# Kernel tuning notes

Measured on AMD Instinct MI355X. Metric: run time of the kernel, lower is better.

The kernel has to match this reference:

```python
import jax, jax.numpy as jnp
import numpy as np

B, S, E, H = 4, 8192, 1024, 16
D = E // H  # head_dim = 64


def setup_inputs() -> dict:
    key = jax.random.key(0)
    ks = jax.random.split(key, 6)
    x = jax.random.normal(ks[0], (B, S, E), dtype=jnp.float32)
    key_padding_mask = jax.random.randint(ks[1], (B, S), 0, 2).astype(jnp.bool_)
    scale = 1.0 / np.sqrt(E)
    Wq = jax.random.normal(ks[2], (E, E), dtype=jnp.float32) * scale
    Wk = jax.random.normal(ks[3], (E, E), dtype=jnp.float32) * scale
    Wv = jax.random.normal(ks[4], (E, E), dtype=jnp.float32) * scale
    Wo = jax.random.normal(ks[5], (E, E), dtype=jnp.float32) * scale
    return {"x": x, "key_padding_mask": key_padding_mask,
            "Wq": Wq, "Wk": Wk, "Wv": Wv, "Wo": Wo}


def reference(x, key_padding_mask, Wq, Wk, Wv, Wo):
    b, s, _ = x.shape
    # torch Linear (no bias): y = x @ W.T
    Q = (x @ Wq.T).reshape(b, s, H, D).transpose(0, 2, 1, 3)  # (b,h,s,d)
    K = (x @ Wk.T).reshape(b, s, H, D).transpose(0, 2, 1, 3)
    V = (x @ Wv.T).reshape(b, s, H, D).transpose(0, 2, 1, 3)
    Q = jax.nn.elu(Q) + 1.0
    K = jax.nn.elu(K) + 1.0
    mask = key_padding_mask[:, None, :, None]  # (b,1,s,1), True = padding
    K = jnp.where(mask, 0.0, K)
    V = jnp.where(mask, 0.0, V)
    # global KV summarization over sequence: (b,h,d,e)
    KV = jnp.einsum('bhsd,bhse->bhde', K, V)
    K_sum = K.sum(axis=2)  # (b,h,d)
    Z = 1.0 / (jnp.einsum('bhsd,bhd->bhs', Q, K_sum) + 1e-6)  # (b,h,s)
    out = jnp.einsum('bhsd,bhde->bhse', Q, KV) * Z[..., None]  # (b,h,s,e)
    out = out.transpose(0, 2, 1, 3).reshape(b, s, E)
    return out @ Wo.T
```

## Files before the change

kernel.cpp:

```cpp
#include <hip/hip_runtime.h>

#define NB 4
#define NS 8192
#define NE 1024
#define NH 16
#define ND 64
#define NM (NB*NS)
#define NKT 16

typedef __bf16 bf16x8 __attribute__((ext_vector_type(8)));
typedef float  f32x4  __attribute__((ext_vector_type(4)));
typedef unsigned short u16x8 __attribute__((ext_vector_type(8)));

__device__ __forceinline__ unsigned short f2bf(float f){
  unsigned int u = __float_as_uint(f);
  u += 0x7FFFu + ((u >> 16) & 1u);
  return (unsigned short)(u >> 16);
}
__device__ __forceinline__ float bf2f(unsigned short h){
  return __uint_as_float(((unsigned int)h) << 16);
}
__device__ __forceinline__ void gload16(const void* g, void* lds){
  __builtin_amdgcn_global_load_lds(
      (__attribute__((address_space(1))) unsigned int*)g,
      (__attribute__((address_space(3))) unsigned int*)lds, 16, 0, 0);
}

__global__ void mask_prep(const void* mraw, unsigned char* mask_u8){
  __shared__ int flag_s;
  if (threadIdx.x == 0) flag_s = 0;
  __syncthreads();
  const unsigned int* mi = (const unsigned int*)mraw;
  int bad = 0;
  for (int i = threadIdx.x; i < 4096; i += 256) bad |= (mi[i] > 1u) ? 1 : 0;
  if (bad) atomicOr(&flag_s, 1);
  __syncthreads();
  const int isbyte = flag_s;
  const unsigned char* mb = (const unsigned char*)mraw;
  int stride = gridDim.x * blockDim.x;
  for (int i = blockIdx.x*blockDim.x + threadIdx.x; i < NM; i += stride)
    mask_u8[i] = isbyte ? (unsigned char)(mb[i] != 0) : (unsigned char)(mi[i] != 0);
}

struct CastJobs {
  const float* src[5];
  unsigned short* dst[5];
  int n4[5];
};

__global__ __launch_bounds__(256) void castk(CastJobs J){
  int j = blockIdx.y;
  const float* s = J.src[j];
  unsigned short* d = J.dst[j];
  int n4 = J.n4[j];
  int stride = gridDim.x * blockDim.x;
  for (int i = blockIdx.x*blockDim.x + threadIdx.x; i < n4; i += stride){
    float4 v = *(const float4*)(s + (long)i*4);
    ushort4 o;
    o.x = f2bf(v.x); o.y = f2bf(v.y); o.z = f2bf(v.z); o.w = f2bf(v.w);
    *(ushort4*)(d + (long)i*4) = o;
  }
}

__global__ __launch_bounds__(512, 2) void gemm256(
    const unsigned short* __restrict__ A,
    const unsigned short* __restrict__ W1,
    const unsigned short* __restrict__ W2,
    unsigned short* __restrict__ O1,
    unsigned short* __restrict__ O2,
    float* __restrict__ OF,
    const unsigned char* __restrict__ mask,
    int modeSel)
{
  __shared__ __align__(16) unsigned short As[2*256*64];
  __shared__ __align__(16) unsigned short Bs[2*256*64];

  const int mode = (modeSel < 0) ? (int)blockIdx.y + 1 : modeSel;
  const unsigned short* Bw = (mode==1) ? W1 : (mode==2) ? W2 : W1;
  unsigned short* Obf = (mode==1) ? O1 : O2;

  const int nwg = (int)gridDim.x;
  const int bx  = (int)blockIdx.x;
  const int swz = (bx & 7) * (nwg >> 3) + (bx >> 3);
  const long m0 = (long)(swz >> 2) * 256;
  const int  n0 = (swz & 3) * 256;

  const int tid = (int)threadIdx.x;
  const int l   = tid & 63;
  const int wv  = tid >> 6;
  const int wr  = wv >> 2;
  const int wc  = wv & 3;
  const int l15 = l & 15;
  const int lhi = l >> 4;
  const int swz8 = (l & 7) * 8;

  const int srow = wv*16 + (l >> 3);
  const int scol = ((l & 7) * 8) ^ ((l >> 3) << 3);

  auto stageA = [&](int st, int h){
    if (st >= NKT) return;
    const long col = (long)st*64 + scol;
    #pragma unroll
    for (int is = 0; is < 2; ++is)
      gload16(A + (m0 + h*128 + srow + is*8)*NE + col,
              &As[(st & 1)*16384 + h*8192 + (wv*2 + is)*512]);
  };
  auto stageB = [&](int st, int h){
    if (st >= NKT) return;
    const long col = (long)st*64 + scol;
    #pragma unroll
    for (int is = 0; is < 2; ++is)
      gload16(Bw + (long)(n0 + h*128 + srow + is*8)*NE + col,
              &Bs[(st & 1)*16384 + h*8192 + (wv*2 + is)*512]);
  };

  auto lda = [&](int buf, int mi, int ks)->bf16x8 {
    const int row = wr*128 + mi*16 + l15;
    const int col = (ks*32 + lhi*8) ^ swz8;
    return *(const bf16x8*)&As[buf*16384 + row*64 + col];
  };
  auto ldb = [&](int buf, int ni, int ks)->bf16x8 {
    const int row = wc*64 + ni*16 + l15;
    const int col = (ks*32 + lhi*8) ^ swz8;
    return *(const bf16x8*)&Bs[buf*16384 + row*64 + col];
  };

  f32x4 acc[8][4];
  #pragma unroll
  for (int i=0;i<8;++i)
    #pragma unroll
    for (int j=0;j<4;++j)
      acc[i][j] = (f32x4){0.f,0.f,0.f,0.f};

  stageA(0,0); stageA(0,1); stageB(0,0); stageB(0,1);
  stageA(1,0); stageA(1,1); stageB(1,0); stageB(1,1);
  asm volatile("s_waitcnt vmcnt(8)" ::: "memory");
  __builtin_amdgcn_s_barrier();

  bf16x8 a0[4][2], a1[4][2], b0[2][2], b1[2][2];

  #pragma unroll 2
  for (int kt = 0; kt < NKT; ++kt){
    const int buf = kt & 1;

    #pragma unroll
    for (int i=0;i<4;++i){ a0[i][0]=lda(buf,i,0); a0[i][1]=lda(buf,i,1); }
    #pragma unroll
    for (int j=0;j<2;++j){ b0[j][0]=ldb(buf,j,0); b0[j][1]=ldb(buf,j,1); }
    asm volatile("s_waitcnt lgkmcnt(0)" ::: "memory");
    __builtin_amdgcn_sched_barrier(0);
    __builtin_amdgcn_s_setprio(1);
    #pragma unroll
    for (int ks=0;ks<2;++ks)
      #pragma unroll
      for (int i=0;i<4;++i)
        #pragma unroll
        for (int j=0;j<2;++j)
          acc[i][j] = __builtin_amdgcn_mfma_f32_16x16x32_bf16(a0[i][ks], b0[j][ks], acc[i][j], 0,0,0);
    __builtin_amdgcn_s_setprio(0);
    __builtin_amdgcn_s_barrier();

    #pragma unroll
    for (int i=0;i<4;++i){ a1[i][0]=lda(buf,4+i,0); a1[i][1]=lda(buf,4+i,1); }
    asm volatile("s_waitcnt lgkmcnt(0)" ::: "memory");
    __builtin_amdgcn_sched_barrier(0);
    __builtin_amdgcn_s_setprio(1);
    #pragma unroll
    for (int ks=0;ks<2;++ks)
      #pragma unroll
      for (int i=0;i<4;++i)
        #pragma unroll
        for (int j=0;j<2;++j)
          acc[4+i][j] = __builtin_amdgcn_mfma_f32_16x16x32_bf16(a1[i][ks], b0[j][ks], acc[4+i][j], 0,0,0);
    __builtin_amdgcn_s_setprio(0);
    __builtin_amdgcn_s_barrier();

    #pragma unroll
    for (int j=0;j<2;++j){ b1[j][0]=ldb(buf,2+j,0); b1[j][1]=ldb(buf,2+j,1); }
    stageA(kt+2, 0); stageA(kt+2, 1);
    asm volatile("s_waitcnt lgkmcnt(0)" ::: "memory");
    __builtin_amdgcn_sched_barrier(0);
    __builtin_amdgcn_s_setprio(1);
    #pragma unroll
    for (int ks=0;ks<2;++ks)
      #pragma unroll
      for (int i=0;i<4;++i)
        #pragma unroll
        for (int j=0;j<2;++j)
          acc[4+i][2+j] = __builtin_amdgcn_mfma_f32_16x16x32_bf16(a1[i][ks], b1[j][ks], acc[4+i][2+j], 0,0,0);
    __builtin_amdgcn_s_setprio(0);
    __builtin_amdgcn_s_barrier();

    stageB(kt+2, 0); stageB(kt+2, 1);
    __builtin_amdgcn_sched_barrier(0);
    __builtin_amdgcn_s_setprio(1);
    #pragma unroll
    for (int ks=0;ks<2;++ks)
      #pragma unroll
      for (int i=0;i<4;++i)
        #pragma unroll
        for (int j=0;j<2;++j)
          acc[i][2+j] = __builtin_amdgcn_mfma_f32_16x16x32_bf16(a0[i][ks], b1[j][ks], acc[i][2+j], 0,0,0);
    __builtin_amdgcn_s_setprio(0);
    if (kt < NKT-2)       asm volatile("s_waitcnt vmcnt(8)" ::: "memory");
    else if (kt == NKT-2) asm volatile("s_waitcnt vmcnt(0)" ::: "memory");
    __builtin_amdgcn_s_barrier();
  }

  #pragma unroll
  for (int mi=0;mi<8;++mi){
    #pragma unroll
    for (int r=0;r<4;++r){
      const long mg = m0 + wr*128 + mi*16 + lhi*4 + r;
      const bool mz = (mode==1 || mode==2) ? (mask[mg] != 0) : false;
      #pragma unroll
      for (int ni=0;ni<4;++ni){
        const int ng = n0 + wc*64 + ni*16 + l15;
        float v = acc[mi][ni][r];
        if (mode==1) v = (v > 0.f) ? (v + 1.f) : __expf(v);
        if (mz) v = 0.f;
        if (mode==3) OF[mg*NE + ng] = v;
        else         Obf[mg*NE + ng] = f2bf(v);
      }
    }
  }
}

__global__ __launch_bounds__(512, 2) void gemm_q_attn(
    const unsigned short* __restrict__ A,
    const unsigned short* __restrict__ Wq,
    const unsigned short* __restrict__ KVfrag,
    unsigned short* __restrict__ attnb)
{
  __shared__ __align__(16) unsigned short As[2*256*64];
  __shared__ __align__(16) unsigned short Bs[2*256*64];

  const int nwg = (int)gridDim.x;
  const int bx  = (int)blockIdx.x;
  const int swz = (bx & 7) * (nwg >> 3) + (bx >> 3);
  const long m0 = (long)(swz >> 2) * 256;
  const int  n0 = (swz & 3) * 256;

  const int tid = (int)threadIdx.x;
  const int l   = tid & 63;
  const int wv  = tid >> 6;
  const int wr  = wv >> 2;
  const int wc  = wv & 3;
  const int l15 = l & 15;
  const int lhi = l >> 4;
  const int swz8 = (l & 7) * 8;

  const int srow = wv*16 + (l >> 3);
  const int scol = ((l & 7) * 8) ^ ((l >> 3) << 3);

  auto stageA = [&](int st, int h){
    if (st >= NKT) return;
    const long col = (long)st*64 + scol;
    #pragma unroll
    for (int is = 0; is < 2; ++is)
      gload16(A + (m0 + h*128 + srow + is*8)*NE + col,
              &As[(st & 1)*16384 + h*8192 + (wv*2 + is)*512]);
  };
  auto stageB = [&](int st, int h){
    if (st >= NKT) return;
    const long col = (long)st*64 + scol;
    #pragma unroll
    for (int is = 0; is < 2; ++is)
      gload16(Wq + (long)(n0 + h*128 + srow + is*8)*NE + col,
              &Bs[(st & 1)*16384 + h*8192 + (wv*2 + is)*512]);
  };

  auto lda = [&](int buf, int mi, int ks)->bf16x8 {
    const int row = wr*128 + mi*16 + l15;
    const int col = (ks*32 + lhi*8) ^ swz8;
    return *(const bf16x8*)&As[buf*16384 + row*64 + col];
  };
  auto ldb = [&](int buf, int ni, int ks)->bf16x8 {
    const int row = wc*64 + ni*16 + l15;
    const int col = (ks*32 + lhi*8) ^ swz8;
    return *(const bf16x8*)&Bs[buf*16384 + row*64 + col];
  };

  f32x4 acc[8][4];
  #pragma unroll
  for (int i=0;i<8;++i)
    #pragma unroll
    for (int j=0;j<4;++j)
      acc[i][j] = (f32x4){0.f,0.f,0.f,0.f};

  stageA(0,0); stageA(0,1); stageB(0,0); stageB(0,1);
  stageA(1,0); stageA(1,1); stageB(1,0); stageB(1,1);
  asm volatile("s_waitcnt vmcnt(8)" ::: "memory");
  __builtin_amdgcn_s_barrier();

  bf16x8 a0[4][2], a1[4][2], b0[2][2], b1[2][2];

  #pragma unroll 2
  for (int kt = 0; kt < NKT; ++kt){
    const int buf = kt & 1;

    #pragma unroll
    for (int i=0;i<4;++i){ a0[i][0]=lda(buf,i,0); a0[i][1]=lda(buf,i,1); }
    #pragma unroll
    for (int j=0;j<2;++j){ b0[j][0]=ldb(buf,j,0); b0[j][1]=ldb(buf,j,1); }
    asm volatile("s_waitcnt lgkmcnt(0)" ::: "memory");
    __builtin_amdgcn_sched_barrier(0);
    __builtin_amdgcn_s_setprio(1);
    #pragma unroll
    for (int ks=0;ks<2;++ks)
      #pragma unroll
      for (int i=0;i<4;++i)
        #pragma unroll
        for (int j=0;j<2;++j)
          acc[i][j] = __builtin_amdgcn_mfma_f32_16x16x32_bf16(a0[i][ks], b0[j][ks], acc[i][j], 0,0,0);
    __builtin_amdgcn_s_setprio(0);
    __builtin_amdgcn_s_barrier();

    #pragma unroll
    for (int i=0;i<4;++i){ a1[i][0]=lda(buf,4+i,0); a1[i][1]=lda(buf,4+i,1); }
    asm volatile("s_waitcnt lgkmcnt(0)" ::: "memory");
    __builtin_amdgcn_sched_barrier(0);
    __builtin_amdgcn_s_setprio(1);
    #pragma unroll
    for (int ks=0;ks<2;++ks)
      #pragma unroll
      for (int i=0;i<4;++i)
        #pragma unroll
        for (int j=0;j<2;++j)
          acc[4+i][j] = __builtin_amdgcn_mfma_f32_16x16x32_bf16(a1[i][ks], b0[j][ks], acc[4+i][j], 0,0,0);
    __builtin_amdgcn_s_setprio(0);
    __builtin_amdgcn_s_barrier();

    #pragma unroll
    for (int j=0;j<2;++j){ b1[j][0]=ldb(buf,2+j,0); b1[j][1]=ldb(buf,2+j,1); }
    stageA(kt+2, 0); stageA(kt+2, 1);
    asm volatile("s_waitcnt lgkmcnt(0)" ::: "memory");
    __builtin_amdgcn_sched_barrier(0);
    __builtin_amdgcn_s_setprio(1);
    #pragma unroll
    for (int ks=0;ks<2;++ks)
      #pragma unroll
      for (int i=0;i<4;++i)
        #pragma unroll
        for (int j=0;j<2;++j)
          acc[4+i][2+j] = __builtin_amdgcn_mfma_f32_16x16x32_bf16(a1[i][ks], b1[j][ks], acc[4+i][2+j], 0,0,0);
    __builtin_amdgcn_s_setprio(0);
    __builtin_amdgcn_s_barrier();

    stageB(kt+2, 0); stageB(kt+2, 1);
    __builtin_amdgcn_sched_barrier(0);
    __builtin_amdgcn_s_setprio(1);
    #pragma unroll
    for (int ks=0;ks<2;++ks)
      #pragma unroll
      for (int i=0;i<4;++i)
        #pragma unroll
        for (int j=0;j<2;++j)
          acc[i][2+j] = __builtin_amdgcn_mfma_f32_16x16x32_bf16(a0[i][ks], b1[j][ks], acc[i][2+j], 0,0,0);
    __builtin_amdgcn_s_setprio(0);
    if (kt < NKT-2)       asm volatile("s_waitcnt vmcnt(8)" ::: "memory");
    else if (kt == NKT-2) asm volatile("s_waitcnt vmcnt(0)" ::: "memory");
    __builtin_amdgcn_s_barrier();
  }

  const int b  = (int)(m0 >> 13);
  const int h  = (swz & 3)*4 + wc;
  const long bh = (long)(b*16 + h);
  unsigned short* pool = (wv < 4) ? &As[wv*8192] : &Bs[(wv-4)*8192];

  #pragma unroll
  for (int mi=0;mi<8;++mi){
    #pragma unroll
    for (int r=0;r<4;++r){
      const int row = mi*16 + lhi*4 + r;
      #pragma unroll
      for (int ni=0;ni<4;++ni){
        float v = acc[mi][ni][r];
        v = (v > 0.f) ? (v + 1.f) : __expf(v);
        const int colb = (ni*16 + l15)*2;
        *(unsigned short*)((char*)pool + row*128 + (colb ^ ((row & 7) << 4))) = f2bf(v);
      }
    }
  }

  bf16x8 bfv[4][5];
  #pragma unroll
  for (int ks=0; ks<4; ++ks)
    #pragma unroll
    for (int nt=0; nt<5; ++nt)
      bfv[ks][nt] = *(const bf16x8*)(KVfrag + bh*10240 + (ks*5+nt)*512 + l*8);

  asm volatile("s_waitcnt lgkmcnt(0)" ::: "memory");
  __builtin_amdgcn_sched_barrier(0);

  const int swzb = (l15 & 7) << 4;
  #pragma unroll
  for (int rt=0; rt<8; ++rt){
    const int rb = (rt*16 + l15)*128;
    bf16x8 qa0 = *(const bf16x8*)((const char*)pool + rb + ((lhi*16) ^ swzb));
    bf16x8 qa1 = *(const bf16x8*)((const char*)pool + rb + ((64 + lhi*16) ^ swzb));
    f32x4 at[5];
    #pragma unroll
    for (int nt=0; nt<5; ++nt){
      at[nt] = (f32x4){0.f,0.f,0.f,0.f};
      at[nt] = __builtin_amdgcn_mfma_f32_16x16x32_bf16(qa0, bfv[0][nt], at[nt], 0,0,0);
      at[nt] = __builtin_amdgcn_mfma_f32_16x16x32_bf16(qa1, bfv[1][nt], at[nt], 0,0,0);
      at[nt] = __builtin_amdgcn_mfma_f32_16x16x32_bf16(qa0, bfv[2][nt], at[nt], 0,0,0);
      at[nt] = __builtin_amdgcn_mfma_f32_16x16x32_bf16(qa1, bfv[3][nt], at[nt], 0,0,0);
    }
    float dv[4];
    #pragma unroll
    for (int e=0;e<4;++e){
      float d = __shfl(at[4][e], l & 48, 64);
      dv[e] = 1.f / (d + 1e-6f);
    }
    #pragma unroll
    for (int nt=0; nt<4; ++nt){
      #pragma unroll
      for (int e=0;e<4;++e){
        const int row = rt*16 + lhi*4 + e;
        const int colb = (nt*16 + l15)*2;
        *(unsigned short*)((char*)pool + row*128 + (colb ^ ((row & 7) << 4))) = f2bf(at[nt][e] * dv[e]);
      }
    }
  }

  asm volatile("s_waitcnt lgkmcnt(0)" ::: "memory");
  __builtin_amdgcn_sched_barrier(0);
  #pragma unroll
  for (int c=0;c<16;++c){
    const int r = c*8 + (l >> 3);
    bf16x8 vv = *(const bf16x8*)((const char*)pool + r*128 + ((((l&7) ^ (r & 7))) << 4));
    *(bf16x8*)(attnb + (m0 + wr*128 + r)*NE + h*ND + (l&7)*8) = vv;
  }
}

__global__ __launch_bounds__(256) void kv_reduce(const unsigned short* __restrict__ K,
                                                 const unsigned short* __restrict__ V,
                                                 float* __restrict__ part){
  __shared__ float lds[2*64*68 + 192];
  float* Ksf = lds;
  float* Vsf = lds + 64*68;
  float* kcorner = lds + 2*64*68;

  const int bid = blockIdx.x;
  const int bh = bid >> 5;
  const int chunk = bid & 31;
  const int b = bh >> 4, h = bh & 15;
  const int t = threadIdx.x, w = t >> 6, l = t & 63;
  const int dg = l & 7, eg = l >> 3;
  const int d0 = dg*8, e0 = eg*8;
  const long base = ((long)b*NS + (long)chunk*256)*NE + h*ND;

  f32x4 acc[8][2];
  #pragma unroll
  for (int j=0;j<8;++j){ acc[j][0]=(f32x4){0,0,0,0}; acc[j][1]=(f32x4){0,0,0,0}; }
  f32x4 ksa = (f32x4){0,0,0,0}, ksb = (f32x4){0,0,0,0};

  for (int sc = 0; sc < 4; ++sc){
    if (sc) __syncthreads();
    const long rbase = base + (long)sc*64*NE;
    #pragma unroll
    for (int p = 0; p < 2; ++p){
      const int g = p*256 + t;
      const int row = g >> 3, cg = (g & 7)*8;
      u16x8 ku = *(const u16x8*)(K + rbase + (long)row*NE + cg);
      u16x8 vu = *(const u16x8*)(V + rbase + (long)row*NE + cg);
      #pragma unroll
      for (int j=0;j<8;++j){
        Ksf[row*68 + cg + j] = bf2f(ku[j]);
        Vsf[row*68 + cg + j] = bf2f(vu[j]);
      }
    }
    __syncthreads();
    #pragma unroll 2
    for (int i = 0; i < 16; ++i){
      const int r = w*16 + i;
      f32x4 k0 = *(const f32x4*)&Ksf[r*68 + d0];
      f32x4 k1 = *(const f32x4*)&Ksf[r*68 + d0 + 4];
      f32x4 v0 = *(const f32x4*)&Vsf[r*68 + e0];
      f32x4 v1 = *(const f32x4*)&Vsf[r*68 + e0 + 4];
      #pragma unroll
      for (int j=0;j<4;++j){
        acc[j][0]   += k0[j]*v0;  acc[j][1]   += k0[j]*v1;
        acc[4+j][0] += k1[j]*v0;  acc[4+j][1] += k1[j]*v1;
      }
      if (eg == 0){ ksa += k0; ksb += k1; }
    }
  }

  __syncthreads();
  if (w >= 1 && eg == 0){
    *(f32x4*)&kcorner[(w-1)*64 + d0]     = ksa;
    *(f32x4*)&kcorner[(w-1)*64 + d0 + 4] = ksb;
  }
  if (w >= 2){
    float* reg = (w==2) ? Ksf : Vsf;
    #pragma unroll
    for (int j=0;j<8;++j)
      #pragma unroll
      for (int q=0;q<2;++q)
        *(f32x4*)&reg[l*68 + (j*2+q)*4] = acc[j][q];
  }
  __syncthreads();
  if (w < 2){
    float* reg = (w==0) ? Ksf : Vsf;
    #pragma unroll
    for (int j=0;j<8;++j)
      #pragma unroll
      for (int q=0;q<2;++q)
        acc[j][q] += *(const f32x4*)&reg[l*68 + (j*2+q)*4];
  }
  __syncthreads();
  if (w == 1){
    #pragma unroll
    for (int j=0;j<8;++j)
      #pragma unroll
      for (int q=0;q<2;++q)
        *(f32x4*)&Ksf[l*68 + (j*2+q)*4] = acc[j][q];
  }
  __syncthreads();
  if (w == 0){
    #pragma unroll
    for (int j=0;j<8;++j)
      #pragma unroll
      for (int q=0;q<2;++q)
        acc[j][q] += *(const f32x4*)&Ksf[l*68 + (j*2+q)*4];
    float* po = part + (long)(bh*32 + chunk)*4160;
    #pragma unroll
    for (int j=0;j<8;++j)
      #pragma unroll
      for (int q=0;q<2;++q)
        *(f32x4*)&po[(d0 + j)*64 + e0 + q*4] = acc[j][q];
    if (eg == 0){
      #pragma unroll
      for (int i=0;i<3;++i){
        ksa += *(const f32x4*)&kcorner[i*64 + d0];
        ksb += *(const f32x4*)&kcorner[i*64 + d0 + 4];
      }
      *(f32x4*)&po[4096 + d0]     = ksa;
      *(f32x4*)&po[4096 + d0 + 4] = ksb;
    }
  }
}

__global__ __launch_bounds__(256) void kv_finish(const float* __restrict__ part,
                                                 unsigned short* __restrict__ KVfrag){
  __shared__ float KVf[64*65 + 32];
  const int bh = blockIdx.x, t = threadIdx.x;
  const float* pb = part + (long)bh*32*4160;

  #pragma unroll
  for (int p = 0; p < 4; ++p){
    int g = p*256 + t;
    f32x4 s = (f32x4){0.f,0.f,0.f,0.f};
    for (int c = 0; c < 32; ++c) s += *(const f32x4*)&pb[c*4160 + g*4];
    int d = g >> 4, e = (g & 15)*4;
    KVf[d*65 + e+0] = s[0];
    KVf[d*65 + e+1] = s[1];
    KVf[d*65 + e+2] = s[2];
    KVf[d*65 + e+3] = s[3];
  }
  if (t < 16){
    f32x4 s = (f32x4){0.f,0.f,0.f,0.f};
    for (int c = 0; c < 32; ++c) s += *(const f32x4*)&pb[c*4160 + 4096 + t*4];
    #pragma unroll
    for (int j=0;j<4;++j) KVf[(t*4+j)*65 + 64] = s[j];
  }
  __syncthreads();

  for (int idx = t; idx < 10240; idx += 256){
    int j   = idx & 7;
    int lfr = (idx >> 3) & 63;
    int grp = idx >> 9;
    int nt  = grp % 5, ks = grp / 5;
    int kk  = (ks & 1)*32 + (lfr >> 4)*8 + j;
    int n   = nt*16 + (lfr & 15);
    float v = (n <= 64) ? KVf[kk*65 + n] : 0.f;
    unsigned short hi = f2bf(v);
    unsigned short o  = (ks >> 1) ? f2bf(v - bf2f(hi)) : hi;
    KVfrag[(long)bh*10240 + idx] = o;
  }
}

extern "C" void kernel_launch(void* const* d_in, const int* in_sizes, int n_in,
                              void* d_out, int out_size, void* d_ws, size_t ws_size,
                              hipStream_t stream){
  (void)in_sizes; (void)n_in; (void)out_size; (void)ws_size;
  const float* x    = (const float*)d_in[0];
  const void*  mraw = d_in[1];
  const float* Wq   = (const float*)d_in[2];
  const float* Wk   = (const float*)d_in[3];
  const float* Wv   = (const float*)d_in[4];
  const float* Wo   = (const float*)d_in[5];
  float* out = (float*)d_out;
  char* ws = (char*)d_ws;

  unsigned short* xb  = (unsigned short*)(ws + 0L);
  unsigned short* Wqb = (unsigned short*)(ws + 67108864L);
  unsigned short* Wkb = (unsigned short*)(ws + 69206016L);
  unsigned short* Wvb = (unsigned short*)(ws + 71303168L);
  unsigned short* Wob = (unsigned short*)(ws + 73400320L);
  unsigned short* Qb  = (unsigned short*)(ws + 75497472L);
  unsigned short* Kb  = (unsigned short*)(ws + 142606336L);
  unsigned short* Vb  = (unsigned short*)(ws + 209715200L);
  unsigned short* KVfrag = (unsigned short*)(ws + 276824064L);
  unsigned char* mask_u8 = (unsigned char*)(ws + 278462464L);
  float* part = (float*)Qb;
  unsigned short* attnb = Qb;

  mask_prep<<<32, 256, 0, stream>>>(mraw, mask_u8);

  CastJobs J;
  J.src[0]=x;  J.dst[0]=xb;  J.n4[0]=NM*NE/4;
  J.src[1]=Wq; J.dst[1]=Wqb; J.n4[1]=NE*NE/4;
  J.src[2]=Wk; J.dst[2]=Wkb; J.n4[2]=NE*NE/4;
  J.src[3]=Wv; J.dst[3]=Wvb; J.n4[3]=NE*NE/4;
  J.src[4]=Wo; J.dst[4]=Wob; J.n4[4]=NE*NE/4;
  castk<<<dim3(2048,5), 256, 0, stream>>>(J);

  gemm256<<<dim3(512,2), 512, 0, stream>>>(xb, Wkb, Wvb, Kb, Vb, nullptr, mask_u8, -1);

  kv_reduce<<<dim3(2048), 256, 0, stream>>>(Kb, Vb, part);
  kv_finish<<<dim3(64), 256, 0, stream>>>(part, KVfrag);

  gemm_q_attn<<<dim3(512), 512, 0, stream>>>(xb, Wqb, KVfrag, attnb);

  gemm256<<<dim3(512,1), 512, 0, stream>>>(attnb, Wob, Wob, nullptr, nullptr, out, mask_u8, 3);
}
```

Before: 456.0 us.

## Replace four-phase interleaved GEMM main loop with single load-then-compute phase

Both GEMM kernels' inner loops move from four ping-pong phases, each loading a quarter of the LDS fragments and issuing a block of MFMAs between barriers, to one phase. That phase loads all A and B fragments, issues the next-tile global-to-LDS staging, then runs all 64 MFMAs per tile. The aim is fewer barriers and lgkmcnt waits per iteration. In exchange, LDS reads no longer overlap with MFMA work, and more fragment registers are live at once, which may raise VGPR pressure and reduce occupancy.

```diff
diff --git a/kernel.cpp b/kernel.cpp
--- a/kernel.cpp
+++ b/kernel.cpp
@@ -137,71 +137,34 @@
   asm volatile("s_waitcnt vmcnt(8)" ::: "memory");
   __builtin_amdgcn_s_barrier();
 
-  bf16x8 a0[4][2], a1[4][2], b0[2][2], b1[2][2];
+  bf16x8 av[8][2], bv[4][2];
 
   #pragma unroll 2
   for (int kt = 0; kt < NKT; ++kt){
     const int buf = kt & 1;
 
     #pragma unroll
-    for (int i=0;i<4;++i){ a0[i][0]=lda(buf,i,0); a0[i][1]=lda(buf,i,1); }
-    #pragma unroll
-    for (int j=0;j<2;++j){ b0[j][0]=ldb(buf,j,0); b0[j][1]=ldb(buf,j,1); }
+    for (int i=0;i<8;++i){ av[i][0]=lda(buf,i,0); av[i][1]=lda(buf,i,1); }
+    #pragma unroll
+    for (int j=0;j<4;++j){ bv[j][0]=ldb(buf,j,0); bv[j][1]=ldb(buf,j,1); }
     asm volatile("s_waitcnt lgkmcnt(0)" ::: "memory");
     __builtin_amdgcn_sched_barrier(0);
-    __builtin_amdgcn_s_setprio(1);
-    #pragma unroll
-    for (int ks=0;ks<2;++ks)
-      #pragma unroll
-      for (int i=0;i<4;++i)
-        #pragma unroll
-        for (int j=0;j<2;++j)
-          acc[i][j] = __builtin_amdgcn_mfma_f32_16x16x32_bf16(a0[i][ks], b0[j][ks], acc[i][j], 0,0,0);
-    __builtin_amdgcn_s_setprio(0);
     __builtin_amdgcn_s_barrier();
 
-    #pragma unroll
-    for (int i=0;i<4;++i){ a1[i][0]=lda(buf,4+i,0); a1[i][1]=lda(buf,4+i,1); }
-    asm volatile("s_waitcnt lgkmcnt(0)" ::: "memory");
-    __builtin_amdgcn_sched_barrier(0);
-    __builtin_amdgcn_s_setprio(1);
-    #pragma unroll
-    for (int ks=0;ks<2;++ks)
-      #pragma unroll
-      for (int i=0;i<4;++i)
-        #pragma unroll
-        for (int j=0;j<2;++j)
-          acc[4+i][j] = __builtin_amdgcn_mfma_f32_16x16x32_bf16(a1[i][ks], b0[j][ks], acc[4+i][j], 0,0,0);
-    __builtin_amdgcn_s_setprio(0);
-    __builtin_amdgcn_s_barrier();
-
-    #pragma unroll
-    for (int j=0;j<2;++j){ b1[j][0]=ldb(buf,2+j,0); b1[j][1]=ldb(buf,2+j,1); }
     stageA(kt+2, 0); stageA(kt+2, 1);
-    asm volatile("s_waitcnt lgkmcnt(0)" ::: "memory");
-    __builtin_amdgcn_sched_barrier(0);
-    __builtin_amdgcn_s_setprio(1);
-    #pragma unroll
-    for (int ks=0;ks<2;++ks)
-      #pragma unroll
-      for (int i=0;i<4;++i)
-        #pragma unroll
-        for (int j=0;j<2;++j)
-          acc[4+i][2+j] = __builtin_amdgcn_mfma_f32_16x16x32_bf16(a1[i][ks], b1[j][ks], acc[4+i][2+j], 0,0,0);
-    __builtin_amdgcn_s_setprio(0);
-    __builtin_amdgcn_s_barrier();
-
     stageB(kt+2, 0); stageB(kt+2, 1);
     __builtin_amdgcn_sched_barrier(0);
+
     __builtin_amdgcn_s_setprio(1);
     #pragma unroll
     for (int ks=0;ks<2;++ks)
       #pragma unroll
-      for (int i=0;i<4;++i)
+      for (int i=0;i<8;++i)
         #pragma unroll
-        for (int j=0;j<2;++j)
-          acc[i][2+j] = __builtin_amdgcn_mfma_f32_16x16x32_bf16(a0[i][ks], b1[j][ks], acc[i][2+j], 0,0,0);
+        for (int j=0;j<4;++j)
+          acc[i][j] = __builtin_amdgcn_mfma_f32_16x16x32_bf16(av[i][ks], bv[j][ks], acc[i][j], 0,0,0);
     __builtin_amdgcn_s_setprio(0);
+
     if (kt < NKT-2)       asm volatile("s_waitcnt vmcnt(8)" ::: "memory");
     else if (kt == NKT-2) asm volatile("s_waitcnt vmcnt(0)" ::: "memory");
     __builtin_amdgcn_s_barrier();
@@ -293,71 +256,34 @@
   asm volatile("s_waitcnt vmcnt(8)" ::: "memory");
   __builtin_amdgcn_s_barrier();
 
-  bf16x8 a0[4][2], a1[4][2], b0[2][2], b1[2][2];
+  bf16x8 av[8][2], bv[4][2];
 
   #pragma unroll 2
   for (int kt = 0; kt < NKT; ++kt){
     const int buf = kt & 1;
 
     #pragma unroll
-    for (int i=0;i<4;++i){ a0[i][0]=lda(buf,i,0); a0[i][1]=lda(buf,i,1); }
-    #pragma unroll
-    for (int j=0;j<2;++j){ b0[j][0]=ldb(buf,j,0); b0[j][1]=ldb(buf,j,1); }
+    for (int i=0;i<8;++i){ av[i][0]=lda(buf,i,0); av[i][1]=lda(buf,i,1); }
+    #pragma unroll
+    for (int j=0;j<4;++j){ bv[j][0]=ldb(buf,j,0); bv[j][1]=ldb(buf,j,1); }
     asm volatile("s_waitcnt lgkmcnt(0)" ::: "memory");
     __builtin_amdgcn_sched_barrier(0);
-    __builtin_amdgcn_s_setprio(1);
-    #pragma unroll
-    for (int ks=0;ks<2;++ks)
-      #pragma unroll
-      for (int i=0;i<4;++i)
-        #pragma unroll
-        for (int j=0;j<2;++j)
-          acc[i][j] = __builtin_amdgcn_mfma_f32_16x16x32_bf16(a0[i][ks], b0[j][ks], acc[i][j], 0,0,0);
-    __builtin_amdgcn_s_setprio(0);
     __builtin_amdgcn_s_barrier();
 
-    #pragma unroll
-    for (int i=0;i<4;++i){ a1[i][0]=lda(buf,4+i,0); a1[i][1]=lda(buf,4+i,1); }
-    asm volatile("s_waitcnt lgkmcnt(0)" ::: "memory");
-    __builtin_amdgcn_sched_barrier(0);
-    __builtin_amdgcn_s_setprio(1);
-    #pragma unroll
-    for (int ks=0;ks<2;++ks)
-      #pragma unroll
-      for (int i=0;i<4;++i)
-        #pragma unroll
-        for (int j=0;j<2;++j)
-          acc[4+i][j] = __builtin_amdgcn_mfma_f32_16x16x32_bf16(a1[i][ks], b0[j][ks], acc[4+i][j], 0,0,0);
-    __builtin_amdgcn_s_setprio(0);
-    __builtin_amdgcn_s_barrier();
-
-    #pragma unroll
-    for (int j=0;j<2;++j){ b1[j][0]=ldb(buf,2+j,0); b1[j][1]=ldb(buf,2+j,1); }
     stageA(kt+2, 0); stageA(kt+2, 1);
-    asm volatile("s_waitcnt lgkmcnt(0)" ::: "memory");
-    __builtin_amdgcn_sched_barrier(0);
-    __builtin_amdgcn_s_setprio(1);
-    #pragma unroll
-    for (int ks=0;ks<2;++ks)
-      #pragma unroll
-      for (int i=0;i<4;++i)
-        #pragma unroll
-        for (int j=0;j<2;++j)
-          acc[4+i][2+j] = __builtin_amdgcn_mfma_f32_16x16x32_bf16(a1[i][ks], b1[j][ks], acc[4+i][2+j], 0,0,0);
-    __builtin_amdgcn_s_setprio(0);
-    __builtin_amdgcn_s_barrier();
-
     stageB(kt+2, 0); stageB(kt+2, 1);
     __builtin_amdgcn_sched_barrier(0);
+
     __builtin_amdgcn_s_setprio(1);
     #pragma unroll
     for (int ks=0;ks<2;++ks)
       #pragma unroll
-      for (int i=0;i<4;++i)
+      for (int i=0;i<8;++i)
         #pragma unroll
-        for (int j=0;j<2;++j)
-          acc[i][2+j] = __builtin_amdgcn_mfma_f32_16x16x32_bf16(a0[i][ks], b1[j][ks], acc[i][2+j], 0,0,0);
+        for (int j=0;j<4;++j)
+          acc[i][j] = __builtin_amdgcn_mfma_f32_16x16x32_bf16(av[i][ks], bv[j][ks], acc[i][j], 0,0,0);
     __builtin_amdgcn_s_setprio(0);
+
     if (kt < NKT-2)       asm volatile("s_waitcnt vmcnt(8)" ::: "memory");
     else if (kt == NKT-2) asm volatile("s_waitcnt vmcnt(0)" ::: "memory");
     __builtin_amdgcn_s_barrier();
```

Measured after the change: 690.7 us. +51.5%, slower.
